# Kernel tuning notes

Hardware: AMD Instinct MI355X
Metric: run time of the kernel (lower is better)

The kernel has to match this reference:

```python
import jax, jax.numpy as jnp
import numpy as np

NEG_BIG = -9e15
ALPHA = 0.2  # LeakyReLU negative slope


def setup_inputs() -> dict:
    key = jax.random.key(0)
    k1, k2, k3, k4 = jax.random.split(key, 4)
    N, Fin, Fout = 8192, 256, 256
    input_ = jax.random.normal(k1, (N, Fin), dtype=jnp.float32)
    adj = jax.random.randint(k2, (N, N), 0, 2, dtype=jnp.int32)
    # xavier_uniform with gain=1.414
    limW = 1.414 * np.sqrt(6.0 / (Fin + Fout))
    W = jax.random.uniform(k3, (Fin, Fout), minval=-limW, maxval=limW, dtype=jnp.float32)
    lima = 1.414 * np.sqrt(6.0 / (2 * Fout + 1))
    a = jax.random.uniform(k4, (2 * Fout, 1), minval=-lima, maxval=lima, dtype=jnp.float32)
    return {"input_": input_, "adj": adj, "W": W, "a": a}


def reference(input_, adj, W, a):
    # h: [N, F]
    h = input_ @ W
    F = h.shape[1]
    # Decompose cat([h_i, h_j]) @ a into per-node projections summed by broadcast
    src = h @ a[:F, 0]   # [N]  contribution of row node i
    dst = h @ a[F:, 0]   # [N]  contribution of col node j
    e = jax.nn.leaky_relu(src[:, None] + dst[None, :], negative_slope=ALPHA)  # [N, N]
    e = jnp.where(adj > 0, e, NEG_BIG)
    attention = jax.nn.softmax(e, axis=1)
    h_prime = attention @ h  # [N, F]
    return jax.nn.relu(h_prime)  # concat=True
```

## Files before the change

kernel.cpp:

```cpp
#include <hip/hip_runtime.h>
#include <math.h>

#define NN 8192
#define FF 256
#define ALPHA 0.2f
#define SS 4
#define JSEG (NN / SS)
#define STEPS (JSEG / 32)

typedef __bf16 bf16x8 __attribute__((ext_vector_type(8)));
typedef __bf16 bf16x4 __attribute__((ext_vector_type(4)));
typedef float  f32x4  __attribute__((ext_vector_type(4)));

__global__ __launch_bounds__(256) void k0_wt(const float* __restrict__ W,
                                             __bf16* __restrict__ WT) {
    __shared__ float ts[64][65];
    const int t = threadIdx.x;
    const int k0 = blockIdx.x * 64;
    const int n0 = blockIdx.y * 64;
    #pragma unroll
    for (int r = 0; r < 4; ++r) {
        int krow = r * 16 + (t >> 4);
        int nc4 = (t & 15) * 4;
        *(float4*)&ts[krow][nc4] = *(const float4*)&W[(size_t)(k0 + krow) * FF + n0 + nc4];
    }
    __syncthreads();
    const int nloc = t >> 2;
    const int kc = (t & 3) * 16;
    union { bf16x8 v[2]; __bf16 e[16]; } hi, lo;
    #pragma unroll
    for (int u = 0; u < 16; ++u) {
        float x = ts[kc + u][nloc];
        __bf16 h1 = (__bf16)x;
        hi.e[u] = h1;
        lo.e[u] = (__bf16)(x - (float)h1);
    }
    size_t base = (size_t)(n0 + nloc) * FF + k0 + kc;
    *(bf16x8*)&WT[base] = hi.v[0];
    *(bf16x8*)&WT[base + 8] = hi.v[1];
    size_t lbase = (size_t)FF * FF + base;
    *(bf16x8*)&WT[lbase] = lo.v[0];
    *(bf16x8*)&WT[lbase + 8] = lo.v[1];
}

__global__ __launch_bounds__(256) void k1_h(const float* __restrict__ X,
                                            const __bf16* __restrict__ WT,
                                            const float* __restrict__ a,
                                            __bf16* __restrict__ hT,
                                            float* __restrict__ src,
                                            float* __restrict__ dst) {
    __shared__ __bf16 ax[2][32][40];
    __shared__ float hs[32][264];
    __shared__ float red[2][4][32];
    const int t = threadIdx.x;
    const int i0 = blockIdx.x * 32;
    const int l = t & 63, wv = t >> 6, ln = l & 15, g = l >> 4;
    f32x4 acc[2][4];
    #pragma unroll
    for (int mt = 0; mt < 2; ++mt)
        #pragma unroll
        for (int nt = 0; nt < 4; ++nt)
            acc[mt][nt] = (f32x4){0.f, 0.f, 0.f, 0.f};

    for (int ks = 0; ks < 8; ++ks) {
        const int k0 = ks * 32;
        {
            int row = t >> 3, c4 = (t & 7) * 4;
            float4 xv = *(const float4*)&X[(size_t)(i0 + row) * FF + k0 + c4];
            bf16x4 hi4, lo4;
            float xs_[4] = {xv.x, xv.y, xv.z, xv.w};
            #pragma unroll
            for (int u = 0; u < 4; ++u) {
                __bf16 h1 = (__bf16)xs_[u];
                hi4[u] = h1;
                lo4[u] = (__bf16)(xs_[u] - (float)h1);
            }
            *(bf16x4*)&ax[0][row][c4] = hi4;
            *(bf16x4*)&ax[1][row][c4] = lo4;
        }
        __syncthreads();
        bf16x8 ah[2], al[2];
        ah[0] = *(bf16x8*)&ax[0][ln][g * 8];
        ah[1] = *(bf16x8*)&ax[0][16 + ln][g * 8];
        al[0] = *(bf16x8*)&ax[1][ln][g * 8];
        al[1] = *(bf16x8*)&ax[1][16 + ln][g * 8];
        #pragma unroll
        for (int nt = 0; nt < 4; ++nt) {
            const int n = wv * 64 + nt * 16 + ln;
            bf16x8 bh8 = *(const bf16x8*)&WT[(size_t)n * FF + k0 + g * 8];
            bf16x8 bl8 = *(const bf16x8*)&WT[(size_t)(FF + n) * FF + k0 + g * 8];
            #pragma unroll
            for (int mt = 0; mt < 2; ++mt) {
                acc[mt][nt] = __builtin_amdgcn_mfma_f32_16x16x32_bf16(ah[mt], bh8, acc[mt][nt], 0, 0, 0);
                acc[mt][nt] = __builtin_amdgcn_mfma_f32_16x16x32_bf16(ah[mt], bl8, acc[mt][nt], 0, 0, 0);
                acc[mt][nt] = __builtin_amdgcn_mfma_f32_16x16x32_bf16(al[mt], bh8, acc[mt][nt], 0, 0, 0);
            }
        }
        __syncthreads();
    }
    float an[4], ad[4];
    #pragma unroll
    for (int nt = 0; nt < 4; ++nt) {
        an[nt] = a[wv * 64 + nt * 16 + ln];
        ad[nt] = a[FF + wv * 64 + nt * 16 + ln];
    }
    float sp[2][4], dp[2][4];
    #pragma unroll
    for (int mt = 0; mt < 2; ++mt)
        #pragma unroll
        for (int rg = 0; rg < 4; ++rg) { sp[mt][rg] = 0.f; dp[mt][rg] = 0.f; }
    #pragma unroll
    for (int mt = 0; mt < 2; ++mt)
        #pragma unroll
        for (int nt = 0; nt < 4; ++nt)
            #pragma unroll
            for (int rg = 0; rg < 4; ++rg) {
                float v = acc[mt][nt][rg];
                hs[mt * 16 + g * 4 + rg][wv * 64 + nt * 16 + ln] = v;
                sp[mt][rg] += v * an[nt];
                dp[mt][rg] += v * ad[nt];
            }
    #pragma unroll
    for (int mk = 1; mk < 16; mk <<= 1)
        #pragma unroll
        for (int mt = 0; mt < 2; ++mt)
            #pragma unroll
            for (int rg = 0; rg < 4; ++rg) {
                sp[mt][rg] += __shfl_xor(sp[mt][rg], mk);
                dp[mt][rg] += __shfl_xor(dp[mt][rg], mk);
            }
    if (ln == 0) {
        #pragma unroll
        for (int mt = 0; mt < 2; ++mt)
            #pragma unroll
            for (int rg = 0; rg < 4; ++rg) {
                red[0][wv][mt * 16 + g * 4 + rg] = sp[mt][rg];
                red[1][wv][mt * 16 + g * 4 + rg] = dp[mt][rg];
            }
    }
    __syncthreads();
    if (t < 32) {
        src[i0 + t] = red[0][0][t] + red[0][1][t] + red[0][2][t] + red[0][3][t];
        dst[i0 + t] = red[1][0][t] + red[1][1][t] + red[1][2][t] + red[1][3][t];
    }
    {
        const int f = t;
        #pragma unroll
        for (int jc = 0; jc < 4; ++jc) {
            union { bf16x8 v; __bf16 e[8]; } hi;
            #pragma unroll
            for (int u = 0; u < 8; ++u) {
                float x = hs[jc * 8 + u][f];
                hi.e[u] = (__bf16)x;
            }
            *(bf16x8*)&hT[(size_t)f * NN + i0 + jc * 8] = hi.v;
        }
    }
}

__global__ __launch_bounds__(256) void k2a_pack(const int* __restrict__ adj,
                                                unsigned* __restrict__ bits) {
    const size_t total4 = (size_t)NN * NN / 4;
    const int l = threadIdx.x & 63;
    const int base = l & 56;
    size_t t = (size_t)blockIdx.x * 256 + threadIdx.x;
    const size_t stride = (size_t)gridDim.x * 256;
    for (; t < total4; t += stride) {
        int4 v = ((const int4*)adj)[t];
        unsigned nib = (unsigned)(v.x > 0) | ((unsigned)(v.y > 0) << 1)
                     | ((unsigned)(v.z > 0) << 2) | ((unsigned)(v.w > 0) << 3);
        unsigned w = 0;
        #pragma unroll
        for (int k = 0; k < 8; ++k)
            w |= (unsigned)__shfl((int)nib, base + k) << (4 * k);
        if ((l & 7) == 0)
            bits[t >> 3] = w;
    }
}

__global__ __launch_bounds__(256) void k2b_max(const float* __restrict__ dst,
                                               float* __restrict__ maxd) {
    __shared__ float red[256];
    float m = -1e30f;
    #pragma unroll
    for (int r = 0; r < NN / 1024; ++r) {
        float4 v = *(const float4*)&dst[(r * 256 + threadIdx.x) * 4];
        m = fmaxf(m, fmaxf(fmaxf(v.x, v.y), fmaxf(v.z, v.w)));
    }
    red[threadIdx.x] = m;
    __syncthreads();
    for (int s = 128; s > 0; s >>= 1) {
        if (threadIdx.x < s) red[threadIdx.x] = fmaxf(red[threadIdx.x], red[threadIdx.x + s]);
        __syncthreads();
    }
    if (threadIdx.x == 0) maxd[0] = red[0];
}

__global__ __launch_bounds__(256, 2) void k3_attn(const unsigned* __restrict__ bits,
                                                  const __bf16* __restrict__ hT,
                                                  const float* __restrict__ src,
                                                  const float* __restrict__ dst,
                                                  const float* __restrict__ maxd,
                                                  float* __restrict__ num,
                                                  float* __restrict__ den) {
    __shared__ __bf16 bh[2][1024 * 8];
    __shared__ unsigned mlds[64 * 68];
    __shared__ float dsts[JSEG];
    const int t = threadIdx.x;
    const int l = t & 63, wv = t >> 6, ln = l & 15, g = l >> 4;
    const int it = blockIdx.x & 127;
    const int seg = blockIdx.x >> 7;
    const int i0 = it * 64;
    const int jbeg = seg * JSEG;
    const int rl = wv * 16 + ln;
    const int row = i0 + rl;
    const float maxdv = maxd[0];
    const float src_r = src[row];
    const float e0 = src_r + maxdv;
    const float m_r = e0 > 0.f ? e0 : ALPHA * e0;

    int ga[4], lc[4];
    #pragma unroll
    for (int r = 0; r < 4; ++r) {
        int c = r * 256 + wv * 64 + l;
        int f = c >> 2;
        int pc = c & 3;
        int jc = pc ^ ((f >> 1) & 3);
        ga[r] = f * NN + jc * 8;
        lc[r] = c * 8;
    }
    const int rb = ln * 64 + ((g ^ ((ln >> 1) & 3)) * 16);
    const char* bh0 = (const char*)&bh[0][0] + rb;
    const char* bh1 = (const char*)&bh[1][0] + rb;

    int4 rA[4], rB[4];
    #pragma unroll
    for (int r = 0; r < 4; ++r) rA[r] = *(const int4*)&hT[ga[r] + jbeg];
    #pragma unroll
    for (int r = 0; r < 4; ++r) rB[r] = *(const int4*)&hT[ga[r] + jbeg + 32];
    {
        int r = t >> 2;
        const int4* gsrc = (const int4*)(bits + (size_t)(i0 + r) * (NN / 32) + (jbeg >> 5));
        int4* ldst = (int4*)&mlds[r * 68];
        #pragma unroll
        for (int u = 0; u < 4; ++u)
            ldst[u * 4 + (t & 3)] = gsrc[u * 4 + (t & 3)];
    }
    #pragma unroll
    for (int u = 0; u < 2; ++u)
        *(float4*)&dsts[(u * 256 + t) * 4] = *(const float4*)&dst[jbeg + (u * 256 + t) * 4];
    #pragma unroll
    for (int r = 0; r < 4; ++r) *(int4*)&bh[0][lc[r]] = rA[r];
    __syncthreads();

    float den_reg = 0.f;
    f32x4 acc[16];
    #pragma unroll
    for (int nt = 0; nt < 16; ++nt) acc[nt] = (f32x4){0.f, 0.f, 0.f, 0.f};

#define K3_WCOMP(S_, AF_)                                                     \
    {                                                                         \
        unsigned mb = (mlds[rl * 68 + (S_)] >> (g * 8)) & 0xffu;              \
        const float* dp_ = &dsts[(S_) * 32 + g * 8];                          \
        float4 dq0 = *(const float4*)dp_;                                     \
        float4 dq1 = *(const float4*)(dp_ + 4);                               \
        const float dv[8] = {dq0.x, dq0.y, dq0.z, dq0.w,                      \
                             dq1.x, dq1.y, dq1.z, dq1.w};                     \
        _Pragma("unroll")                                                     \
        for (int u = 0; u < 8; ++u) {                                         \
            float e = src_r + dv[u];                                          \
            e = e > 0.f ? e : ALPHA * e;                                      \
            float ex = __expf(e - m_r);                                       \
            float w = (mb & (1u << u)) ? ex : 0.f;                            \
            den_reg += w;                                                     \
            AF_.e[u] = (__bf16)w;                                             \
        }                                                                     \
    }

#define K3_MFMA(AF_, BP_)                                                     \
    {                                                                         \
        _Pragma("unroll")                                                     \
        for (int nt = 0; nt < 16; ++nt) {                                     \
            bf16x8 bfr = *(const bf16x8*)((BP_) + nt * 1024);                 \
            acc[nt] = __builtin_amdgcn_mfma_f32_16x16x32_bf16(                \
                AF_.v, bfr, acc[nt], 0, 0, 0);                                \
        }                                                                     \
    }

    for (int s = 0; s < STEPS; s += 2) {
        if (s + 2 < STEPS) {
            #pragma unroll
            for (int r = 0; r < 4; ++r)
                rA[r] = *(const int4*)&hT[ga[r] + jbeg + (s + 2) * 32];
        }
        union { bf16x8 v; __bf16 e[8]; } afe;
        K3_WCOMP(s, afe);
        #pragma unroll
        for (int r = 0; r < 4; ++r) *(int4*)&bh[1][lc[r]] = rB[r];
        K3_MFMA(afe, bh0);
        __syncthreads();
        if (s + 3 < STEPS) {
            #pragma unroll
            for (int r = 0; r < 4; ++r)
                rB[r] = *(const int4*)&hT[ga[r] + jbeg + (s + 3) * 32];
        }
        union { bf16x8 v; __bf16 e[8]; } afo;
        K3_WCOMP(s + 1, afo);
        if (s + 2 < STEPS) {
            #pragma unroll
            for (int r = 0; r < 4; ++r) *(int4*)&bh[0][lc[r]] = rA[r];
        }
        K3_MFMA(afo, bh1);
        __syncthreads();
    }
    den_reg += __shfl_xor(den_reg, 16);
    den_reg += __shfl_xor(den_reg, 32);
    if (g == 0) den[(size_t)seg * NN + row] = den_reg;
    #pragma unroll
    for (int nt = 0; nt < 16; ++nt)
        #pragma unroll
        for (int rg = 0; rg < 4; ++rg)
            num[((size_t)seg * NN + i0 + wv * 16 + g * 4 + rg) * FF
                + nt * 16 + ln] = acc[nt][rg];
}

__global__ __launch_bounds__(256) void k4_out(const float* __restrict__ num,
                                              const float* __restrict__ den,
                                              float* __restrict__ out) {
    size_t f4 = (size_t)blockIdx.x * 256 + threadIdx.x;
    int i = (int)(f4 >> 6);
    int c4 = (int)(f4 & 63) << 2;
    float4 s = make_float4(0.f, 0.f, 0.f, 0.f);
    float d = 0.f;
    #pragma unroll
    for (int sg = 0; sg < SS; ++sg) {
        float4 v = *(const float4*)&num[((size_t)sg * NN + i) * FF + c4];
        s.x += v.x; s.y += v.y; s.z += v.z; s.w += v.w;
        d += den[(size_t)sg * NN + i];
    }
    float inv = 1.f / d;
    float4 o;
    o.x = fmaxf(s.x * inv, 0.f);
    o.y = fmaxf(s.y * inv, 0.f);
    o.z = fmaxf(s.z * inv, 0.f);
    o.w = fmaxf(s.w * inv, 0.f);
    *(float4*)&out[(size_t)i * FF + c4] = o;
}

extern "C" void kernel_launch(void* const* d_in, const int* in_sizes, int n_in,
                              void* d_out, int out_size, void* d_ws, size_t ws_size,
                              hipStream_t stream) {
    const float* X  = (const float*)d_in[0];
    const int*  adj = (const int*)d_in[1];
    const float* W  = (const float*)d_in[2];
    const float* a  = (const float*)d_in[3];
    float* out = (float*)d_out;
    char* ws = (char*)d_ws;

    const size_t off_hT   = 0;
    const size_t off_wt   = off_hT + (size_t)FF * NN * 2;
    const size_t off_src  = off_wt + (size_t)2 * FF * FF * 2;
    const size_t off_dst  = off_src + (size_t)NN * 4;
    const size_t off_maxd = off_dst + (size_t)NN * 4;
    const size_t off_num  = off_maxd + 256;
    const size_t off_den  = off_num + (size_t)SS * NN * FF * 4;
    const size_t off_bits = off_den + (size_t)SS * NN * 4;

    __bf16* hT_ws = (__bf16*)(ws + off_hT);
    __bf16* wt_ws = (__bf16*)(ws + off_wt);
    float* src_ws = (float*)(ws + off_src);
    float* dst_ws = (float*)(ws + off_dst);
    float* maxd   = (float*)(ws + off_maxd);
    float* num_ws = (float*)(ws + off_num);
    float* den_ws = (float*)(ws + off_den);
    unsigned* bits_ws = (unsigned*)(ws + off_bits);

    k2a_pack<<<2048, 256, 0, stream>>>(adj, bits_ws);
    k0_wt<<<dim3(FF / 64, FF / 64), 256, 0, stream>>>(W, wt_ws);
    k1_h<<<NN / 32, 256, 0, stream>>>(X, wt_ws, a, hT_ws, src_ws, dst_ws);
    k2b_max<<<1, 256, 0, stream>>>(dst_ws, maxd);
    k3_attn<<<(NN / 64) * SS, 256, 0, stream>>>(bits_ws, hT_ws, src_ws, dst_ws, maxd,
                                                num_ws, den_ws);
    k4_out<<<(NN * FF / 4) / 256, 256, 0, stream>>>(num_ws, den_ws, out);
}
```

Measured before the change: 512.4 us.

## Stream hT tiles via global_load_lds, drop mask LDS, double j-splits and occupancy

Measured after the change: 455.4 us. 1.13x faster.

```diff
diff --git a/kernel.cpp b/kernel.cpp
--- a/kernel.cpp
+++ b/kernel.cpp
@@ -4,13 +4,24 @@
 #define NN 8192
 #define FF 256
 #define ALPHA 0.2f
-#define SS 4
+#define SS 8
 #define JSEG (NN / SS)
 #define STEPS (JSEG / 32)
 
 typedef __bf16 bf16x8 __attribute__((ext_vector_type(8)));
 typedef __bf16 bf16x4 __attribute__((ext_vector_type(4)));
 typedef float  f32x4  __attribute__((ext_vector_type(4)));
+
+__device__ __forceinline__ void dma16(const void* g, void* l) {
+    __builtin_amdgcn_global_load_lds((const __attribute__((address_space(1))) void*)g,
+                                     (__attribute__((address_space(3))) void*)l,
+                                     16, 0, 0);
+}
+
+#define VMCNT0   asm volatile("s_waitcnt vmcnt(0)" ::: "memory")
+#define LGKM0    asm volatile("s_waitcnt lgkmcnt(0)" ::: "memory")
+#define BARRIER  asm volatile("s_barrier" ::: "memory")
+#define FENCE    asm volatile("" ::: "memory")
 
 __global__ __launch_bounds__(256) void k0_wt(const float* __restrict__ W,
                                              __bf16* __restrict__ WT) {
@@ -196,7 +207,7 @@
     if (threadIdx.x == 0) maxd[0] = red[0];
 }
 
-__global__ __launch_bounds__(256, 2) void k3_attn(const unsigned* __restrict__ bits,
+__global__ __launch_bounds__(256, 4) void k3_attn(const unsigned* __restrict__ bits,
                                                   const __bf16* __restrict__ hT,
                                                   const float* __restrict__ src,
                                                   const float* __restrict__ dst,
@@ -204,7 +215,6 @@
                                                   float* __restrict__ num,
                                                   float* __restrict__ den) {
     __shared__ __bf16 bh[2][1024 * 8];
-    __shared__ unsigned mlds[64 * 68];
     __shared__ float dsts[JSEG];
     const int t = threadIdx.x;
     const int l = t & 63, wv = t >> 6, ln = l & 15, g = l >> 4;
@@ -219,38 +229,30 @@
     const float e0 = src_r + maxdv;
     const float m_r = e0 > 0.f ? e0 : ALPHA * e0;
 
-    int ga[4], lc[4];
+    int ga[4], cb[4];
     #pragma unroll
     for (int r = 0; r < 4; ++r) {
-        int c = r * 256 + wv * 64 + l;
+        int cbase = r * 256 + wv * 64;
+        int c = cbase + l;
         int f = c >> 2;
         int pc = c & 3;
         int jc = pc ^ ((f >> 1) & 3);
         ga[r] = f * NN + jc * 8;
-        lc[r] = c * 8;
+        cb[r] = __builtin_amdgcn_readfirstlane(cbase);
     }
     const int rb = ln * 64 + ((g ^ ((ln >> 1) & 3)) * 16);
     const char* bh0 = (const char*)&bh[0][0] + rb;
     const char* bh1 = (const char*)&bh[1][0] + rb;
 
-    int4 rA[4], rB[4];
-    #pragma unroll
-    for (int r = 0; r < 4; ++r) rA[r] = *(const int4*)&hT[ga[r] + jbeg];
-    #pragma unroll
-    for (int r = 0; r < 4; ++r) rB[r] = *(const int4*)&hT[ga[r] + jbeg + 32];
-    {
-        int r = t >> 2;
-        const int4* gsrc = (const int4*)(bits + (size_t)(i0 + r) * (NN / 32) + (jbeg >> 5));
-        int4* ldst = (int4*)&mlds[r * 68];
-        #pragma unroll
-        for (int u = 0; u < 4; ++u)
-            ldst[u * 4 + (t & 3)] = gsrc[u * 4 + (t & 3)];
-    }
-    #pragma unroll
-    for (int u = 0; u < 2; ++u)
-        *(float4*)&dsts[(u * 256 + t) * 4] = *(const float4*)&dst[jbeg + (u * 256 + t) * 4];
-    #pragma unroll
-    for (int r = 0; r < 4; ++r) *(int4*)&bh[0][lc[r]] = rA[r];
+    const unsigned* grow = bits + (size_t)row * (NN / 32) + (jbeg >> 5);
+
+    #pragma unroll
+    for (int r = 0; r < 4; ++r)
+        dma16(&hT[ga[r] + jbeg], &bh[0][cb[r] * 8]);
+    FENCE;
+    *(float4*)&dsts[t * 4] = *(const float4*)&dst[jbeg + t * 4];
+    uint2 wp = *(const uint2*)&grow[0];
+    uint2 wpn = wp;
     __syncthreads();
 
     float den_reg = 0.f;
@@ -258,9 +260,9 @@
     #pragma unroll
     for (int nt = 0; nt < 16; ++nt) acc[nt] = (f32x4){0.f, 0.f, 0.f, 0.f};
 
-#define K3_WCOMP(S_, AF_)                                                     \
+#define K3_WCOMP(S_, MW_, AF_)                                                \
     {                                                                         \
-        unsigned mb = (mlds[rl * 68 + (S_)] >> (g * 8)) & 0xffu;              \
+        unsigned mb = ((MW_) >> (g * 8)) & 0xffu;                             \
         const float* dp_ = &dsts[(S_) * 32 + g * 8];                          \
         float4 dq0 = *(const float4*)dp_;                                     \
         float4 dq1 = *(const float4*)(dp_ + 4);                               \
@@ -288,30 +290,27 @@
     }
 
     for (int s = 0; s < STEPS; s += 2) {
-        if (s + 2 < STEPS) {
+        union { bf16x8 v; __bf16 e[8]; } afe;
+        K3_WCOMP(s, wp.x, afe);
+        FENCE; VMCNT0; LGKM0; BARRIER;
+        #pragma unroll
+        for (int r = 0; r < 4; ++r)
+            dma16(&hT[ga[r] + jbeg + (s + 1) * 32], &bh[1][cb[r] * 8]);
+        if (s + 2 < STEPS) wpn = *(const uint2*)&grow[s + 2];
+        FENCE;
+        K3_MFMA(afe, bh0);
+        union { bf16x8 v; __bf16 e[8]; } afo;
+        K3_WCOMP(s + 1, wp.y, afo);
+        FENCE; VMCNT0; LGKM0; BARRIER;
+        {
+            int sn = (s + 2 < STEPS) ? s + 2 : 0;
             #pragma unroll
             for (int r = 0; r < 4; ++r)
-                rA[r] = *(const int4*)&hT[ga[r] + jbeg + (s + 2) * 32];
+                dma16(&hT[ga[r] + jbeg + sn * 32], &bh[0][cb[r] * 8]);
         }
-        union { bf16x8 v; __bf16 e[8]; } afe;
-        K3_WCOMP(s, afe);
-        #pragma unroll
-        for (int r = 0; r < 4; ++r) *(int4*)&bh[1][lc[r]] = rB[r];
-        K3_MFMA(afe, bh0);
-        __syncthreads();
-        if (s + 3 < STEPS) {
-            #pragma unroll
-            for (int r = 0; r < 4; ++r)
-                rB[r] = *(const int4*)&hT[ga[r] + jbeg + (s + 3) * 32];
-        }
-        union { bf16x8 v; __bf16 e[8]; } afo;
-        K3_WCOMP(s + 1, afo);
-        if (s + 2 < STEPS) {
-            #pragma unroll
-            for (int r = 0; r < 4; ++r) *(int4*)&bh[0][lc[r]] = rA[r];
-        }
+        FENCE;
         K3_MFMA(afo, bh1);
-        __syncthreads();
+        wp = wpn;
     }
     den_reg += __shfl_xor(den_reg, 16);
     den_reg += __shfl_xor(den_reg, 32);
```
